# Optimization experiments

Measured on AMD Instinct MI355X. Metric: run time of the kernel, lower is better.

The kernel has to match this reference:

```python
import jax, jax.numpy as jnp
import numpy as np

B, TGT, SRC = 16, 1024, 1024
TGT_DIM, SRC_DIM = 1024, 1024


def setup_inputs() -> dict:
    key = jax.random.key(0)
    k1, k2, k3, k4 = jax.random.split(key, 4)
    source = jax.random.normal(k1, (B, TGT, TGT_DIM), dtype=jnp.float32)
    memory_bank = jax.random.normal(k2, (B, SRC, SRC_DIM), dtype=jnp.float32)
    # lengths in [1, SRC] so every row has at least one valid position
    memory_lengths = jax.random.randint(k3, (B,), 1, SRC + 1)
    # nn.Linear(tgt_enc_dim, src_enc_dim, bias=False): weight [src_dim, tgt_dim]
    W_in = jax.random.normal(k4, (SRC_DIM, TGT_DIM), dtype=jnp.float32) / np.sqrt(TGT_DIM)
    return {"source": source, "memory_bank": memory_bank,
            "memory_lengths": memory_lengths, "W_in": W_in}


def reference(source, memory_bank, memory_lengths, W_in):
    # general attention: score = (h_t W_in^T) @ h_s^T
    h_t = jnp.einsum('btd,ed->bte', source, W_in)          # [B, TGT, SRC_DIM]
    align = jnp.einsum('bte,bse->bts', h_t, memory_bank)   # [B, TGT, SRC]
    # sequence mask: valid where j < length
    valid = jnp.arange(SRC)[None, :] < memory_lengths[:, None]  # [B, SRC]
    align = jnp.where(valid[:, None, :], align, -jnp.inf)
    return jax.nn.softmax(align, axis=-1)                  # [B, TGT, SRC]
```

## Files before the change

kernel.cpp:

```cpp
#include <hip/hip_runtime.h>
#include <hip/hip_bf16.h>

typedef __bf16 bf16;
typedef __bf16 bf16x8 __attribute__((ext_vector_type(8)));
typedef __bf16 bf16x4 __attribute__((ext_vector_type(4)));
typedef float  f32x4  __attribute__((ext_vector_type(4)));

#define BM 128
#define BN 128
#define BK 32
#define LDK 40

__global__ __launch_bounds__(256) void gemm_bt_split(
    const float* __restrict__ A, const float* __restrict__ Bmat,
    float* __restrict__ C, int M, int N, int K,
    long sAz, long sBz, long sCz)
{
    __shared__ __align__(16) bf16 Ah[BM][LDK];
    __shared__ __align__(16) bf16 Al[BM][LDK];
    __shared__ __align__(16) bf16 Bh[BN][LDK];
    __shared__ __align__(16) bf16 Bl[BN][LDK];

    const int tid  = threadIdx.x;
    const int lane = tid & 63;
    const int wid  = tid >> 6;
    const int wm   = wid >> 1;
    const int wn   = wid & 1;
    const int z    = blockIdx.z;
    const long aBase = (long)z * sAz;
    const long bBase = (long)z * sBz;
    const long cBase = (long)z * sCz;
    const int m0 = blockIdx.x * BM;
    const int n0 = blockIdx.y * BN;

    f32x4 acc[4][4];
#pragma unroll
    for (int i = 0; i < 4; ++i)
#pragma unroll
        for (int j = 0; j < 4; ++j) acc[i][j] = (f32x4)0.0f;

    const int lr = lane & 15;
    const int lk = (lane >> 4) * 8;

    for (int kt = 0; kt < K; kt += BK) {
        __syncthreads();
#pragma unroll
        for (int j = 0; j < 4; ++j) {
            const int idx = j * 256 + tid;
            const int r   = idx >> 3;
            const int c   = (idx & 7) * 4;
            const float4 va = *(const float4*)(A    + aBase + (long)(m0 + r) * K + kt + c);
            const float4 vb = *(const float4*)(Bmat + bBase + (long)(n0 + r) * K + kt + c);

            bf16x4 ah, al, bh, bl;
            ah.x = (bf16)va.x; al.x = (bf16)(va.x - (float)ah.x);
            ah.y = (bf16)va.y; al.y = (bf16)(va.y - (float)ah.y);
            ah.z = (bf16)va.z; al.z = (bf16)(va.z - (float)ah.z);
            ah.w = (bf16)va.w; al.w = (bf16)(va.w - (float)ah.w);
            bh.x = (bf16)vb.x; bl.x = (bf16)(vb.x - (float)bh.x);
            bh.y = (bf16)vb.y; bl.y = (bf16)(vb.y - (float)bh.y);
            bh.z = (bf16)vb.z; bl.z = (bf16)(vb.z - (float)bh.z);
            bh.w = (bf16)vb.w; bl.w = (bf16)(vb.w - (float)bh.w);

            *(bf16x4*)&Ah[r][c] = ah;
            *(bf16x4*)&Al[r][c] = al;
            *(bf16x4*)&Bh[r][c] = bh;
            *(bf16x4*)&Bl[r][c] = bl;
        }
        __syncthreads();

        bf16x8 afh[4], afl[4], bfh[4], bfl[4];
#pragma unroll
        for (int i = 0; i < 4; ++i) {
            afh[i] = *(const bf16x8*)&Ah[wm * 64 + i * 16 + lr][lk];
            afl[i] = *(const bf16x8*)&Al[wm * 64 + i * 16 + lr][lk];
            bfh[i] = *(const bf16x8*)&Bh[wn * 64 + i * 16 + lr][lk];
            bfl[i] = *(const bf16x8*)&Bl[wn * 64 + i * 16 + lr][lk];
        }
#pragma unroll
        for (int i = 0; i < 4; ++i)
#pragma unroll
            for (int j = 0; j < 4; ++j) {
                acc[i][j] = __builtin_amdgcn_mfma_f32_16x16x32_bf16(afh[i], bfh[j], acc[i][j], 0, 0, 0);
                acc[i][j] = __builtin_amdgcn_mfma_f32_16x16x32_bf16(afl[i], bfh[j], acc[i][j], 0, 0, 0);
                acc[i][j] = __builtin_amdgcn_mfma_f32_16x16x32_bf16(afh[i], bfl[j], acc[i][j], 0, 0, 0);
            }
    }

    const int rrow = (lane >> 4) * 4;
#pragma unroll
    for (int i = 0; i < 4; ++i)
#pragma unroll
        for (int j = 0; j < 4; ++j)
#pragma unroll
            for (int q = 0; q < 4; ++q) {
                C[cBase + (long)(m0 + wm * 64 + i * 16 + rrow + q) * N
                        + (n0 + wn * 64 + j * 16 + (lane & 15))] = acc[i][j][q];
            }
}

__global__ __launch_bounds__(256) void softmax_mask_rows(
    float* __restrict__ data, const int* __restrict__ lens, int SRCn, int TGTn)
{
    const int row = blockIdx.x;
    const int b   = row / TGTn;
    const int len = lens[b];
    float* p = data + (long)row * SRCn;

    const int tid  = threadIdx.x;
    const int base = tid * 4;
    const int lane = tid & 63;
    const int wid  = tid >> 6;

    float4 v = *(const float4*)(p + base);
    float vals[4] = {v.x, v.y, v.z, v.w};

    float m = -INFINITY;
#pragma unroll
    for (int j = 0; j < 4; ++j)
        if (base + j < len) m = fmaxf(m, vals[j]);
#pragma unroll
    for (int off = 32; off >= 1; off >>= 1) m = fmaxf(m, __shfl_xor(m, off));

    __shared__ float redm[4];
    __shared__ float reds[4];
    if (lane == 0) redm[wid] = m;
    __syncthreads();
    m = fmaxf(fmaxf(redm[0], redm[1]), fmaxf(redm[2], redm[3]));

    float e[4];
    float s = 0.0f;
#pragma unroll
    for (int j = 0; j < 4; ++j) {
        e[j] = (base + j < len) ? __expf(vals[j] - m) : 0.0f;
        s += e[j];
    }
#pragma unroll
    for (int off = 32; off >= 1; off >>= 1) s += __shfl_xor(s, off);
    if (lane == 0) reds[wid] = s;
    __syncthreads();
    s = reds[0] + reds[1] + reds[2] + reds[3];

    const float inv = 1.0f / s;
    float4 o;
    o.x = e[0] * inv; o.y = e[1] * inv; o.z = e[2] * inv; o.w = e[3] * inv;
    *(float4*)(p + base) = o;
}

extern "C" void kernel_launch(void* const* d_in, const int* in_sizes, int n_in,
                              void* d_out, int out_size, void* d_ws, size_t ws_size,
                              hipStream_t stream)
{
    const float* source         = (const float*)d_in[0];
    const float* memory_bank    = (const float*)d_in[1];
    const int*   memory_lengths = (const int*)  d_in[2];
    const float* W_in           = (const float*)d_in[3];
    float* out = (float*)d_out;
    float* ht  = (float*)d_ws;

    const int Bb = 16, TGT = 1024, SRC = 1024, TD = 1024, SD = 1024;
    dim3 blk(256, 1, 1);

    gemm_bt_split<<<dim3((Bb * TGT) / BM, SD / BN, 1), blk, 0, stream>>>(
        source, W_in, ht, Bb * TGT, SD, TD, 0, 0, 0);

    gemm_bt_split<<<dim3(TGT / BM, SRC / BN, Bb), blk, 0, stream>>>(
        ht, memory_bank, out, TGT, SRC, SD,
        (long)TGT * SD, (long)SRC * SD, (long)TGT * SRC);

    softmax_mask_rows<<<dim3(Bb * TGT, 1, 1), blk, 0, stream>>>(out, memory_lengths, SRC, TGT);
}
```

Measured before the change: 402.5 us.

## Pre-split operands to bf16 hi/lo, load via global_load_lds, swizzle blocks

Adds separate kernels that split fp32 operands into bf16 high/low pairs once. The GEMMs then stream those pairs straight into LDS with global_load_lds instead of converting per tile, and the first GEMM emits its output already split. It also remaps block order for L2 locality and replaces the softmax with one row per wave, avoiding shared-memory reductions. The aim is to cut redundant conversion work and load latency, at the cost of extra split passes, more workspace traffic and unpadded LDS rows that may cause bank conflicts.

```diff
diff --git a/kernel.cpp b/kernel.cpp
--- a/kernel.cpp
+++ b/kernel.cpp
@@ -6,20 +6,237 @@
 typedef __bf16 bf16x4 __attribute__((ext_vector_type(4)));
 typedef float  f32x4  __attribute__((ext_vector_type(4)));
 
-#define BM 128
-#define BN 128
-#define BK 32
-#define LDK 40
+struct hl { bf16 h, l; };
+__device__ __forceinline__ hl split1(float v) {
+    hl r;
+    r.h = (bf16)v;
+    r.l = (bf16)(v - (float)r.h);
+    return r;
+}
+
+__device__ __forceinline__ void glds16(const void* g, void* l) {
+    __builtin_amdgcn_global_load_lds(
+        (const __attribute__((address_space(1))) void*)g,
+        (__attribute__((address_space(3))) void*)l, 16, 0, 0);
+}
+
+template<int AMODE, int BMODE, int OMODE>
+__global__ __launch_bounds__(256) void gemm3(
+    const float* __restrict__ Af, const bf16* __restrict__ Agh, const bf16* __restrict__ Agl,
+    const float* __restrict__ Bf, const bf16* __restrict__ Bgh, const bf16* __restrict__ Bgl,
+    float* __restrict__ Cf, bf16* __restrict__ Cgh, bf16* __restrict__ Cgl,
+    int M, int N, int K, long sAz, long sBz, long sCz, int nbm, int nbn)
+{
+    constexpr int LDA = AMODE ? 32 : 40;
+    constexpr int LDB = BMODE ? 32 : 40;
+    __shared__ __align__(16) bf16 Ah[128 * LDA];
+    __shared__ __align__(16) bf16 Al[128 * LDA];
+    __shared__ __align__(16) bf16 Bh[128 * LDB];
+    __shared__ __align__(16) bf16 Bl[128 * LDB];
+
+    const int tid  = threadIdx.x;
+    const int lane = tid & 63;
+    const int wid  = tid >> 6;
+    const int wm   = wid >> 1;
+    const int wn   = wid & 1;
+
+    const int qq = gridDim.x >> 3;
+    const int sw = (blockIdx.x & 7) * qq + (blockIdx.x >> 3);
+    const int z  = sw / (nbm * nbn);
+    const int tt = sw % (nbm * nbn);
+    const int m0 = (tt / nbn) * 128;
+    const int n0 = (tt % nbn) * 128;
+
+    const float* aF[4]; const float* bF[4];
+    const bf16 *aH0, *aH1, *aL0, *aL1, *bH0, *bH1, *bL0, *bL1;
+    if constexpr (AMODE == 0) {
+#pragma unroll
+        for (int j = 0; j < 4; ++j) {
+            const int idx = j * 256 + tid;
+            aF[j] = Af + (long)z * sAz + (long)(m0 + (idx >> 3)) * K + (idx & 7) * 4;
+        }
+    } else {
+        const int r0 = tid >> 2, c0 = (tid & 3) * 8;
+        aH0 = Agh + (long)z * sAz + (long)(m0 + r0) * K + c0;
+        aH1 = aH0 + (long)64 * K;
+        aL0 = Agl + (long)z * sAz + (long)(m0 + r0) * K + c0;
+        aL1 = aL0 + (long)64 * K;
+    }
+    if constexpr (BMODE == 0) {
+#pragma unroll
+        for (int j = 0; j < 4; ++j) {
+            const int idx = j * 256 + tid;
+            bF[j] = Bf + (long)z * sBz + (long)(n0 + (idx >> 3)) * K + (idx & 7) * 4;
+        }
+    } else {
+        const int r0 = tid >> 2, c0 = (tid & 3) * 8;
+        bH0 = Bgh + (long)z * sBz + (long)(n0 + r0) * K + c0;
+        bH1 = bH0 + (long)64 * K;
+        bL0 = Bgl + (long)z * sBz + (long)(n0 + r0) * K + c0;
+        bL1 = bL0 + (long)64 * K;
+    }
+
+    f32x4 acc[4][4];
+#pragma unroll
+    for (int i = 0; i < 4; ++i)
+#pragma unroll
+        for (int j = 0; j < 4; ++j) acc[i][j] = (f32x4)0.0f;
+
+    const int lr = lane & 15;
+    const int lk = (lane >> 4) * 8;
+
+    for (int kt = 0; kt < K; kt += 32) {
+        __syncthreads();
+        if constexpr (AMODE == 1) {
+            glds16(aH0, &Ah[tid * 8]); glds16(aH1, &Ah[(256 + tid) * 8]);
+            glds16(aL0, &Al[tid * 8]); glds16(aL1, &Al[(256 + tid) * 8]);
+            aH0 += 32; aH1 += 32; aL0 += 32; aL1 += 32;
+        } else {
+#pragma unroll
+            for (int j = 0; j < 4; ++j) {
+                const int idx = j * 256 + tid;
+                const int r = idx >> 3, c = (idx & 7) * 4;
+                const float4 v = *(const float4*)aF[j]; aF[j] += 32;
+                bf16x4 h, l;
+                hl s0 = split1(v.x); h.x = s0.h; l.x = s0.l;
+                hl s1 = split1(v.y); h.y = s1.h; l.y = s1.l;
+                hl s2 = split1(v.z); h.z = s2.h; l.z = s2.l;
+                hl s3 = split1(v.w); h.w = s3.h; l.w = s3.l;
+                *(bf16x4*)&Ah[r * LDA + c] = h;
+                *(bf16x4*)&Al[r * LDA + c] = l;
+            }
+        }
+        if constexpr (BMODE == 1) {
+            glds16(bH0, &Bh[tid * 8]); glds16(bH1, &Bh[(256 + tid) * 8]);
+            glds16(bL0, &Bl[tid * 8]); glds16(bL1, &Bl[(256 + tid) * 8]);
+            bH0 += 32; bH1 += 32; bL0 += 32; bL1 += 32;
+        } else {
+#pragma unroll
+            for (int j = 0; j < 4; ++j) {
+                const int idx = j * 256 + tid;
+                const int r = idx >> 3, c = (idx & 7) * 4;
+                const float4 v = *(const float4*)bF[j]; bF[j] += 32;
+                bf16x4 h, l;
+                hl s0 = split1(v.x); h.x = s0.h; l.x = s0.l;
+                hl s1 = split1(v.y); h.y = s1.h; l.y = s1.l;
+                hl s2 = split1(v.z); h.z = s2.h; l.z = s2.l;
+                hl s3 = split1(v.w); h.w = s3.h; l.w = s3.l;
+                *(bf16x4*)&Bh[r * LDB + c] = h;
+                *(bf16x4*)&Bl[r * LDB + c] = l;
+            }
+        }
+        __syncthreads();
+
+        bf16x8 afh[4], afl[4], bfh[4], bfl[4];
+#pragma unroll
+        for (int i = 0; i < 4; ++i) {
+            afh[i] = *(const bf16x8*)&Ah[(wm * 64 + i * 16 + lr) * LDA + lk];
+            afl[i] = *(const bf16x8*)&Al[(wm * 64 + i * 16 + lr) * LDA + lk];
+            bfh[i] = *(const bf16x8*)&Bh[(wn * 64 + i * 16 + lr) * LDB + lk];
+            bfl[i] = *(const bf16x8*)&Bl[(wn * 64 + i * 16 + lr) * LDB + lk];
+        }
+#pragma unroll
+        for (int i = 0; i < 4; ++i)
+#pragma unroll
+            for (int j = 0; j < 4; ++j) {
+                acc[i][j] = __builtin_amdgcn_mfma_f32_16x16x32_bf16(afh[i], bfh[j], acc[i][j], 0, 0, 0);
+                acc[i][j] = __builtin_amdgcn_mfma_f32_16x16x32_bf16(afl[i], bfh[j], acc[i][j], 0, 0, 0);
+                acc[i][j] = __builtin_amdgcn_mfma_f32_16x16x32_bf16(afh[i], bfl[j], acc[i][j], 0, 0, 0);
+            }
+    }
+
+    const int rr = (lane >> 4) * 4;
+#pragma unroll
+    for (int i = 0; i < 4; ++i)
+#pragma unroll
+        for (int j = 0; j < 4; ++j)
+#pragma unroll
+            for (int q = 0; q < 4; ++q) {
+                const long off = (long)z * sCz
+                               + (long)(m0 + wm * 64 + i * 16 + rr + q) * N
+                               + (n0 + wn * 64 + j * 16 + (lane & 15));
+                if constexpr (OMODE == 0) {
+                    Cf[off] = acc[i][j][q];
+                } else {
+                    hl s = split1(acc[i][j][q]);
+                    Cgh[off] = s.h; Cgl[off] = s.l;
+                }
+            }
+}
+
+__global__ __launch_bounds__(256) void split_pair(
+    const float* __restrict__ x, bf16* __restrict__ h, bf16* __restrict__ l, long n4)
+{
+    long i = (long)blockIdx.x * 256 + threadIdx.x;
+    const long stride = (long)gridDim.x * 256;
+    for (; i < n4; i += stride) {
+        const float4 v = ((const float4*)x)[i];
+        bf16x4 hh, ll;
+        hl s0 = split1(v.x); hh.x = s0.h; ll.x = s0.l;
+        hl s1 = split1(v.y); hh.y = s1.h; ll.y = s1.l;
+        hl s2 = split1(v.z); hh.z = s2.h; ll.z = s2.l;
+        hl s3 = split1(v.w); hh.w = s3.h; ll.w = s3.l;
+        ((bf16x4*)h)[i] = hh;
+        ((bf16x4*)l)[i] = ll;
+    }
+}
+
+__global__ __launch_bounds__(256) void softmax_wave(
+    float* __restrict__ data, const int* __restrict__ lens)
+{
+    const int tid  = threadIdx.x;
+    const int lane = tid & 63;
+    const int row  = blockIdx.x * 4 + (tid >> 6);
+    const int len  = lens[row >> 10];
+    float* p = data + (long)row * 1024;
+
+    float4 v[4];
+#pragma unroll
+    for (int q = 0; q < 4; ++q) v[q] = *(const float4*)(p + 4 * (lane + 64 * q));
+
+    float m = -INFINITY;
+#pragma unroll
+    for (int q = 0; q < 4; ++q) {
+        const int base = 4 * (lane + 64 * q);
+        if (base + 0 < len) m = fmaxf(m, v[q].x);
+        if (base + 1 < len) m = fmaxf(m, v[q].y);
+        if (base + 2 < len) m = fmaxf(m, v[q].z);
+        if (base + 3 < len) m = fmaxf(m, v[q].w);
+    }
+#pragma unroll
+    for (int off = 32; off >= 1; off >>= 1) m = fmaxf(m, __shfl_xor(m, off));
+
+    float s = 0.0f;
+    float4 e[4];
+#pragma unroll
+    for (int q = 0; q < 4; ++q) {
+        const int base = 4 * (lane + 64 * q);
+        e[q].x = (base + 0 < len) ? __expf(v[q].x - m) : 0.0f;
+        e[q].y = (base + 1 < len) ? __expf(v[q].y - m) : 0.0f;
+        e[q].z = (base + 2 < len) ? __expf(v[q].z - m) : 0.0f;
+        e[q].w = (base + 3 < len) ? __expf(v[q].w - m) : 0.0f;
+        s += e[q].x + e[q].y + e[q].z + e[q].w;
+    }
+#pragma unroll
+    for (int off = 32; off >= 1; off >>= 1) s += __shfl_xor(s, off);
+
+    const float inv = 1.0f / s;
+#pragma unroll
+    for (int q = 0; q < 4; ++q) {
+        float4 o; o.x = e[q].x * inv; o.y = e[q].y * inv; o.z = e[q].z * inv; o.w = e[q].w * inv;
+        *(float4*)(p + 4 * (lane + 64 * q)) = o;
+    }
+}
 
 __global__ __launch_bounds__(256) void gemm_bt_split(
     const float* __restrict__ A, const float* __restrict__ Bmat,
     float* __restrict__ C, int M, int N, int K,
     long sAz, long sBz, long sCz)
 {
-    __shared__ __align__(16) bf16 Ah[BM][LDK];
-    __shared__ __align__(16) bf16 Al[BM][LDK];
-    __shared__ __align__(16) bf16 Bh[BN][LDK];
-    __shared__ __align__(16) bf16 Bl[BN][LDK];
+    __shared__ __align__(16) bf16 Ah[128][40];
+    __shared__ __align__(16) bf16 Al[128][40];
+    __shared__ __align__(16) bf16 Bh[128][40];
+    __shared__ __align__(16) bf16 Bl[128][40];
 
     const int tid  = threadIdx.x;
     const int lane = tid & 63;
@@ -30,8 +247,8 @@
     const long aBase = (long)z * sAz;
     const long bBase = (long)z * sBz;
     const long cBase = (long)z * sCz;
-    const int m0 = blockIdx.x * BM;
-    const int n0 = blockIdx.y * BN;
+    const int m0 = blockIdx.x * 128;
+    const int n0 = blockIdx.y * 128;
 
     f32x4 acc[4][4];
 #pragma unroll
@@ -42,7 +259,7 @@
     const int lr = lane & 15;
     const int lk = (lane >> 4) * 8;
 
-    for (int kt = 0; kt < K; kt += BK) {
+    for (int kt = 0; kt < K; kt += 32) {
         __syncthreads();
 #pragma unroll
         for (int j = 0; j < 4; ++j) {
@@ -51,21 +268,17 @@
             const int c   = (idx & 7) * 4;
             const float4 va = *(const float4*)(A    + aBase + (long)(m0 + r) * K + kt + c);
             const float4 vb = *(const float4*)(Bmat + bBase + (long)(n0 + r) * K + kt + c);
-
             bf16x4 ah, al, bh, bl;
-            ah.x = (bf16)va.x; al.x = (bf16)(va.x - (float)ah.x);
-            ah.y = (bf16)va.y; al.y = (bf16)(va.y - (float)ah.y);
-            ah.z = (bf16)va.z; al.z = (bf16)(va.z - (float)ah.z);
-            ah.w = (bf16)va.w; al.w = (bf16)(va.w - (float)ah.w);
-            bh.x = (bf16)vb.x; bl.x = (bf16)(vb.x - (float)bh.x);
-            bh.y = (bf16)vb.y; bl.y = (bf16)(vb.y - (float)bh.y);
-            bh.z = (bf16)vb.z; bl.z = (bf16)(vb.z - (float)bh.z);
-            bh.w = (bf16)vb.w; bl.w = (bf16)(vb.w - (float)bh.w);
-
-            *(bf16x4*)&Ah[r][c] = ah;
-            *(bf16x4*)&Al[r][c] = al;
-            *(bf16x4*)&Bh[r][c] = bh;
-            *(bf16x4*)&Bl[r][c] = bl;
+            hl a0 = split1(va.x); ah.x = a0.h; al.x = a0.l;
+            hl a1 = split1(va.y); ah.y = a1.h; al.y = a1.l;
+            hl a2 = split1(va.z); ah.z = a2.h; al.z = a2.l;
+            hl a3 = split1(va.w); ah.w = a3.h; al.w = a3.l;
+            hl b0 = split1(vb.x); bh.x = b0.h; bl.x = b0.l;
+            hl b1 = split1(vb.y); bh.y = b1.h; bl.y = b1.l;
+            hl b2 = split1(vb.z); bh.z = b2.h; bl.z = b2.l;
+            hl b3 = split1(vb.w); bh.w = b3.h; bl.w = b3.l;
+            *(bf16x4*)&Ah[r][c] = ah; *(bf16x4*)&Al[r][c] = al;
+            *(bf16x4*)&Bh[r][c] = bh; *(bf16x4*)&Bl[r][c] = bl;
         }
         __syncthreads();
 
@@ -87,64 +300,15 @@
             }
     }
 
-    const int rrow = (lane >> 4) * 4;
+    const int rr = (lane >> 4) * 4;
 #pragma unroll
     for (int i = 0; i < 4; ++i)
 #pragma unroll
         for (int j = 0; j < 4; ++j)
 #pragma unroll
-            for (int q = 0; q < 4; ++q) {
-                C[cBase + (long)(m0 + wm * 64 + i * 16 + rrow + q) * N
+            for (int q = 0; q < 4; ++q)
+                C[cBase + (long)(m0 + wm * 64 + i * 16 + rr + q) * N
                         + (n0 + wn * 64 + j * 16 + (lane & 15))] = acc[i][j][q];
-            }
-}
-
-__global__ __launch_bounds__(256) void softmax_mask_rows(
-    float* __restrict__ data, const int* __restrict__ lens, int SRCn, int TGTn)
-{
-    const int row = blockIdx.x;
-    const int b   = row / TGTn;
-    const int len = lens[b];
-    float* p = data + (long)row * SRCn;
-
-    const int tid  = threadIdx.x;
-    const int base = tid * 4;
-    const int lane = tid & 63;
-    const int wid  = tid >> 6;
-
-    float4 v = *(const float4*)(p + base);
-    float vals[4] = {v.x, v.y, v.z, v.w};
-
-    float m = -INFINITY;
-#pragma unroll
-    for (int j = 0; j < 4; ++j)
-        if (base + j < len) m = fmaxf(m, vals[j]);
-#pragma unroll
-    for (int off = 32; off >= 1; off >>= 1) m = fmaxf(m, __shfl_xor(m, off));
-
-    __shared__ float redm[4];
-    __shared__ float reds[4];
-    if (lane == 0) redm[wid] = m;
-    __syncthreads();
-    m = fmaxf(fmaxf(redm[0], redm[1]), fmaxf(redm[2], redm[3]));
-
-    float e[4];
-    float s = 0.0f;
-#pragma unroll
-    for (int j = 0; j < 4; ++j) {
-        e[j] = (base + j < len) ? __expf(vals[j] - m) : 0.0f;
-        s += e[j];
-    }
-#pragma unroll
-    for (int off = 32; off >= 1; off >>= 1) s += __shfl_xor(s, off);
-    if (lane == 0) reds[wid] = s;
-    __syncthreads();
-    s = reds[0] + reds[1] + reds[2] + reds[3];
-
-    const float inv = 1.0f / s;
-    float4 o;
-    o.x = e[0] * inv; o.y = e[1] * inv; o.z = e[2] * inv; o.w = e[3] * inv;
-    *(float4*)(p + base) = o;
 }
 
 extern "C" void kernel_launch(void* const* d_in, const int* in_sizes, int n_in,
@@ -156,17 +320,48 @@
     const int*   memory_lengths = (const int*)  d_in[2];
     const float* W_in           = (const float*)d_in[3];
     float* out = (float*)d_out;
-    float* ht  = (float*)d_ws;
-
-    const int Bb = 16, TGT = 1024, SRC = 1024, TD = 1024, SD = 1024;
-    dim3 blk(256, 1, 1);
-
-    gemm_bt_split<<<dim3((Bb * TGT) / BM, SD / BN, 1), blk, 0, stream>>>(
-        source, W_in, ht, Bb * TGT, SD, TD, 0, 0, 0);
-
-    gemm_bt_split<<<dim3(TGT / BM, SRC / BN, Bb), blk, 0, stream>>>(
-        ht, memory_bank, out, TGT, SRC, SD,
-        (long)TGT * SD, (long)SRC * SD, (long)TGT * SRC);
-
-    softmax_mask_rows<<<dim3(Bb * TGT, 1, 1), blk, 0, stream>>>(out, memory_lengths, SRC, TGT);
-}
+    char*  ws  = (char*)d_ws;
+
+    const size_t MB = 1ull << 20;
+    const long Z = 1024 * 1024;
+
+    if (ws_size >= 197 * MB) {
+        bf16* htH = (bf16*)(ws);            bf16* htL = (bf16*)(ws + 32 * MB);
+        bf16* WH  = (bf16*)(ws + 64 * MB);  bf16* WL  = (bf16*)(ws + 66 * MB);
+        bf16* mbH = (bf16*)(ws + 68 * MB);  bf16* mbL = (bf16*)(ws + 100 * MB);
+        bf16* srH = (bf16*)(ws + 132 * MB); bf16* srL = (bf16*)(ws + 164 * MB);
+        split_pair<<<512,  256, 0, stream>>>(W_in,        WH,  WL,  (1l  << 20) / 4);
+        split_pair<<<2048, 256, 0, stream>>>(memory_bank, mbH, mbL, (16l << 20) / 4);
+        split_pair<<<2048, 256, 0, stream>>>(source,      srH, srL, (16l << 20) / 4);
+        gemm3<1,1,1><<<1024, 256, 0, stream>>>(nullptr, srH, srL, nullptr, WH, WL,
+            nullptr, htH, htL, 16384, 1024, 1024, 0, 0, 0, 128, 8);
+        gemm3<1,1,0><<<1024, 256, 0, stream>>>(nullptr, htH, htL, nullptr, mbH, mbL,
+            out, nullptr, nullptr, 1024, 1024, 1024, Z, Z, Z, 8, 8);
+    } else if (ws_size >= 133 * MB) {
+        bf16* htH = (bf16*)(ws);            bf16* htL = (bf16*)(ws + 32 * MB);
+        bf16* WH  = (bf16*)(ws + 64 * MB);  bf16* WL  = (bf16*)(ws + 66 * MB);
+        bf16* mbH = (bf16*)(ws + 68 * MB);  bf16* mbL = (bf16*)(ws + 100 * MB);
+        split_pair<<<512,  256, 0, stream>>>(W_in,        WH,  WL,  (1l  << 20) / 4);
+        split_pair<<<2048, 256, 0, stream>>>(memory_bank, mbH, mbL, (16l << 20) / 4);
+        gemm3<0,1,1><<<1024, 256, 0, stream>>>(source, nullptr, nullptr, nullptr, WH, WL,
+            nullptr, htH, htL, 16384, 1024, 1024, 0, 0, 0, 128, 8);
+        gemm3<1,1,0><<<1024, 256, 0, stream>>>(nullptr, htH, htL, nullptr, mbH, mbL,
+            out, nullptr, nullptr, 1024, 1024, 1024, Z, Z, Z, 8, 8);
+    } else if (ws_size >= 69 * MB) {
+        bf16* htH = (bf16*)(ws);            bf16* htL = (bf16*)(ws + 32 * MB);
+        bf16* WH  = (bf16*)(ws + 64 * MB);  bf16* WL  = (bf16*)(ws + 66 * MB);
+        split_pair<<<512, 256, 0, stream>>>(W_in, WH, WL, (1l << 20) / 4);
+        gemm3<0,1,1><<<1024, 256, 0, stream>>>(source, nullptr, nullptr, nullptr, WH, WL,
+            nullptr, htH, htL, 16384, 1024, 1024, 0, 0, 0, 128, 8);
+        gemm3<1,0,0><<<1024, 256, 0, stream>>>(nullptr, htH, htL, memory_bank, nullptr, nullptr,
+            out, nullptr, nullptr, 1024, 1024, 1024, Z, Z, Z, 8, 8);
+    } else {
+        float* ht = (float*)ws;
+        gemm_bt_split<<<dim3(128, 8, 1), 256, 0, stream>>>(
+            source, W_in, ht, 16384, 1024, 1024, 0, 0, 0);
+        gemm_bt_split<<<dim3(8, 8, 16), 256, 0, stream>>>(
+            ht, memory_bank, out, 1024, 1024, 1024, Z, Z, Z);
+    }
+
+    softmax_wave<<<4096, 256, 0, stream>>>(out, memory_lengths);
+}
```

After: 422.9 us. 1.05x slower.
